# Kernel optimization log

Hardware: AMD Instinct MI355X
Metric: run time of the kernel (lower is better)

The kernel has to match this reference:

```python
import jax, jax.numpy as jnp
import numpy as np
import math

_OFFSETS = sorted(set(range(0, 33)) | {48, 64, 96, 128, 192, 256, 384, 512, 768, 1024, 1536})
B, N, D, H, FFN = 1, 2048, 1024, 16, 2816
EPS = 1e-6


def _rmsnorm(x, scale):
    rms = jnp.sqrt(jnp.mean(x * x, axis=-1, keepdims=True) + EPS)
    return scale * (x / rms)


def setup_inputs() -> dict:
    key = jax.random.key(0)
    ks = jax.random.split(key, 8)
    s = 0.02
    alphas = jnp.linspace(0.2, 2.0, H)
    delta_vals = jnp.array([math.log(1.0 + max(d, 0.2)) for d in _OFFSETS], dtype=jnp.float32)
    pos_bias = -delta_vals[:, None] * alphas[None, :]  # (n_offsets, H)
    return {
        "x": jax.random.normal(ks[0], (B, N, D), jnp.float32),
        "norm1_scale": jnp.ones((D,), jnp.float32),
        "norm2_scale": jnp.ones((D,), jnp.float32),
        "w_qkv": jax.random.normal(ks[1], (D, 3 * D), jnp.float32) * s,
        "w_out": jax.random.normal(ks[2], (D, D), jnp.float32) * s,
        "w_gate": jax.random.normal(ks[3], (D, D), jnp.float32) * s,
        "b_gate": jnp.full((D,), 2.0, jnp.float32),
        "pos_bias": pos_bias,
        "w_ffn_gate": jax.random.normal(ks[4], (D, FFN), jnp.float32) * s,
        "w_ffn_up": jax.random.normal(ks[5], (D, FFN), jnp.float32) * s,
        "w_ffn_down": jax.random.normal(ks[6], (FFN, D), jnp.float32) * s,
        "offsets": jnp.array(_OFFSETS, dtype=jnp.int32),
    }


def reference(x, norm1_scale, norm2_scale, w_qkv, w_out, w_gate, b_gate,
              pos_bias, w_ffn_gate, w_ffn_up, w_ffn_down, offsets):
    Bx, Nx, Dx = x.shape
    HD = Dx // H
    # --- attention branch: x + attn(norm1(x)) ---
    xn = _rmsnorm(x, norm1_scale)
    qkv = xn @ w_qkv
    q, k, v = jnp.split(qkv, 3, axis=-1)
    to_heads = lambda t: t.reshape(Bx, Nx, H, HD).transpose(0, 2, 1, 3)  # (B,H,N,HD)
    q, k, v = to_heads(q), to_heads(k), to_heads(v)

    t_idx = jnp.arange(Nx)
    # gather positions t-delta per (query t, offset o); clamped positions are masked below
    src = jnp.clip(t_idx[:, None] - offsets[None, :], 0, None)  # (N, O)
    Kg = k[:, :, src, :]  # (B,H,N,O,HD)
    Vg = v[:, :, src, :]

    scale = HD ** (-0.5)
    scores = jnp.einsum('bhnd,bhnod->bhno', q, Kg) * scale
    scores = scores + pos_bias.T[None, :, None, :]  # (1,H,1,O)
    invalid = t_idx[:, None] < offsets[None, :]      # (N, O)
    scores = jnp.where(invalid[None, None], -jnp.inf, scores)
    alpha = jax.nn.softmax(scores, axis=-1)
    out = jnp.einsum('bhno,bhnod->bhnd', alpha, Vg)
    out = out.transpose(0, 2, 1, 3).reshape(Bx, Nx, Dx)

    gate = jax.nn.sigmoid(xn @ w_gate + b_gate)
    x = x + (out * gate) @ w_out

    # --- FFN branch: x + SwiGLU(norm2(x)) ---
    xn2 = _rmsnorm(x, norm2_scale)
    x = x + (jax.nn.silu(xn2 @ w_ffn_gate) * (xn2 @ w_ffn_up)) @ w_ffn_down
    return x
```

## Files before the change

kernel.cpp:

```cpp
#include <hip/hip_runtime.h>
#include <hip/hip_bf16.h>
#include <math.h>

typedef __bf16 bf16;
typedef __bf16 v8bf __attribute__((ext_vector_type(8)));
typedef __bf16 v4bf __attribute__((ext_vector_type(4)));
typedef float v4f __attribute__((ext_vector_type(4)));

#define N_TOK 2048
#define DIM 1024
#define NH 16
#define FFN_DIM 2816

#define GLL(g, l) __builtin_amdgcn_global_load_lds(                         \
    (const __attribute__((address_space(1))) uint32_t*)(g),                 \
    (__attribute__((address_space(3))) uint32_t*)(l), 16, 0, 0)

#define WAITV(n) do {                                                        \
    switch (n) {                                                             \
    case 0: asm volatile("s_waitcnt vmcnt(0)" ::: "memory"); break;          \
    case 2: asm volatile("s_waitcnt vmcnt(2)" ::: "memory"); break;          \
    case 3: asm volatile("s_waitcnt vmcnt(3)" ::: "memory"); break;          \
    case 4: asm volatile("s_waitcnt vmcnt(4)" ::: "memory"); break;          \
    case 6: asm volatile("s_waitcnt vmcnt(6)" ::: "memory"); break;          \
    case 8: asm volatile("s_waitcnt vmcnt(8)" ::: "memory"); break;          \
    default: asm volatile("s_waitcnt vmcnt(0)" ::: "memory"); break; }       \
} while (0)

__global__ __launch_bounds__(256) void prep_all_kernel(
    const float* __restrict__ w_qkv, const float* __restrict__ w_gate,
    const float* __restrict__ w_out, const float* __restrict__ w_ffng,
    const float* __restrict__ w_ffnu, const float* __restrict__ w_ffnd,
    bf16* __restrict__ wqkvgT, bf16* __restrict__ woutT,
    bf16* __restrict__ wcatT, bf16* __restrict__ wffndT,
    const float* __restrict__ x, const float* __restrict__ n1s,
    bf16* __restrict__ xnb)
{
    int bid = blockIdx.x;
    const int tid = threadIdx.x;
    if (bid >= 13568) {
        int row = bid - 13568;
        float4 v = ((const float4*)(x + (size_t)row * DIM))[tid];
        float ss = v.x * v.x + v.y * v.y + v.z * v.z + v.w * v.w;
#pragma unroll
        for (int off = 32; off > 0; off >>= 1) ss += __shfl_down(ss, off);
        __shared__ float ps[4];
        if ((tid & 63) == 0) ps[tid >> 6] = ss;
        __syncthreads();
        float tot = ps[0] + ps[1] + ps[2] + ps[3];
        float inv = rsqrtf(tot * (1.0f / DIM) + 1e-6f);
        float4 s = ((const float4*)n1s)[tid];
        union { bf16 b[4]; uint2 u; } p;
        p.b[0] = (bf16)(v.x * inv * s.x);
        p.b[1] = (bf16)(v.y * inv * s.y);
        p.b[2] = (bf16)(v.z * inv * s.z);
        p.b[3] = (bf16)(v.w * inv * s.w);
        ((uint2*)(xnb + (size_t)row * DIM))[tid] = p.u;
        return;
    }
    const float* W; bf16* D; int Kd, Nc, nb, kb, dstbase;
    if (bid < 3072) {
        W = w_qkv; D = wqkvgT; Kd = 1024; Nc = 3072;
        nb = (bid % 96) * 32; kb = (bid / 96) * 32; dstbase = nb;
    } else if (bid < 4096) { int b = bid - 3072;
        W = w_gate; D = wqkvgT; Kd = 1024; Nc = 1024;
        nb = (b % 32) * 32; kb = (b / 32) * 32; dstbase = 3072 + nb;
    } else if (bid < 5120) { int b = bid - 4096;
        W = w_out; D = woutT; Kd = 1024; Nc = 1024;
        nb = (b % 32) * 32; kb = (b / 32) * 32; dstbase = nb;
    } else if (bid < 7936) { int b = bid - 5120;
        W = w_ffng; D = wcatT; Kd = 1024; Nc = 2816;
        nb = (b % 88) * 32; kb = (b / 88) * 32;
        dstbase = (nb >> 6) * 128 + (nb & 63);
    } else if (bid < 10752) { int b = bid - 7936;
        W = w_ffnu; D = wcatT; Kd = 1024; Nc = 2816;
        nb = (b % 88) * 32; kb = (b / 88) * 32;
        dstbase = (nb >> 6) * 128 + 64 + (nb & 63);
    } else { int b = bid - 10752;
        W = w_ffnd; D = wffndT; Kd = 2816; Nc = 1024;
        nb = (b % 32) * 32; kb = (b / 32) * 32; dstbase = nb;
    }
    __shared__ float tile[32][33];
    int tx = tid & 31, ty = tid >> 5;
#pragma unroll
    for (int r = 0; r < 4; ++r)
        tile[ty + r * 8][tx] = W[(size_t)(kb + ty + r * 8) * Nc + nb + tx];
    __syncthreads();
#pragma unroll
    for (int r = 0; r < 4; ++r)
        D[(size_t)(dstbase + ty + r * 8) * Kd + kb + tx] = (bf16)tile[tx][ty + r * 8];
}

__global__ __launch_bounds__(256) void rmsnorm_kernel(
    const float* __restrict__ x, const float* __restrict__ scale, bf16* __restrict__ out)
{
    int row = blockIdx.x, tid = threadIdx.x;
    float4 v = ((const float4*)(x + (size_t)row * DIM))[tid];
    float ss = v.x * v.x + v.y * v.y + v.z * v.z + v.w * v.w;
#pragma unroll
    for (int off = 32; off > 0; off >>= 1) ss += __shfl_down(ss, off);
    __shared__ float ps[4];
    if ((tid & 63) == 0) ps[tid >> 6] = ss;
    __syncthreads();
    float tot = ps[0] + ps[1] + ps[2] + ps[3];
    float inv = rsqrtf(tot * (1.0f / DIM) + 1e-6f);
    float4 s = ((const float4*)scale)[tid];
    union { bf16 b[4]; uint2 u; } p;
    p.b[0] = (bf16)(v.x * inv * s.x);
    p.b[1] = (bf16)(v.y * inv * s.y);
    p.b[2] = (bf16)(v.z * inv * s.z);
    p.b[3] = (bf16)(v.w * inv * s.w);
    ((uint2*)(out + (size_t)row * DIM))[tid] = p.u;
}

__global__ __launch_bounds__(256) void attn_kernel(
    const bf16* __restrict__ qkvg, const int* __restrict__ offs,
    const float* __restrict__ pos_bias, bf16* __restrict__ attgb)
{
    constexpr int O = 44;
    const int t = blockIdx.x, tid = threadIdx.x;
    const int wv = tid >> 6, lane = tid & 63;
    const int h1 = lane >> 2, l4 = lane & 3;
    const size_t RS = 4 * DIM;
    __shared__ float sS[O][17];
    __shared__ float sPB[O * 16];
    __shared__ int so[O];
    __shared__ float sAcc[4 * 1024];
    if (tid < O) so[tid] = offs[tid];
    for (int i = tid; i < O * 16; i += 256) sPB[i] = pos_bias[i];
    __syncthreads();

    const bf16* qbase = qkvg + (size_t)t * RS + h1 * 64;
    v8bf q0v = *(const v8bf*)(qbase + l4 * 8);
    v8bf q1v = *(const v8bf*)(qbase + 32 + l4 * 8);
    float qa[16];
#pragma unroll
    for (int e = 0; e < 8; ++e) {
        qa[e] = (float)q0v[e] * 0.125f;
        qa[8 + e] = (float)q1v[e] * 0.125f;
    }

#pragma unroll 4
    for (int it = 0; it < 11; ++it) {
        const int o = it * 4 + wv;
        const int src = t - so[o];
        const int srcc = src < 0 ? 0 : src;
        const bf16* kbase = qkvg + (size_t)srcc * RS + DIM + h1 * 64;
        v8bf k0 = *(const v8bf*)(kbase + l4 * 8);
        v8bf k1 = *(const v8bf*)(kbase + 32 + l4 * 8);
        float p = 0.f;
#pragma unroll
        for (int e = 0; e < 8; ++e) p += qa[e] * (float)k0[e];
#pragma unroll
        for (int e = 0; e < 8; ++e) p += qa[8 + e] * (float)k1[e];
        p += __shfl_xor(p, 1);
        p += __shfl_xor(p, 2);
        float s = (src >= 0) ? p + sPB[o * NH + h1] : -INFINITY;
        if (l4 == 0) sS[o][h1] = s;
    }
    __syncthreads();

    const int h = tid >> 4, j16 = tid & 15;
    float mx = -INFINITY;
#pragma unroll
    for (int o = j16; o < O; o += 16) mx = fmaxf(mx, sS[o][h]);
    mx = fmaxf(mx, __shfl_xor(mx, 1));
    mx = fmaxf(mx, __shfl_xor(mx, 2));
    mx = fmaxf(mx, __shfl_xor(mx, 4));
    mx = fmaxf(mx, __shfl_xor(mx, 8));
    float sum = 0.f;
#pragma unroll
    for (int o = j16; o < O; o += 16) {
        float e = __expf(sS[o][h] - mx);
        sS[o][h] = e;
        sum += e;
    }
    sum += __shfl_xor(sum, 1);
    sum += __shfl_xor(sum, 2);
    sum += __shfl_xor(sum, 4);
    sum += __shfl_xor(sum, 8);
    float inv = 1.0f / sum;
    __syncthreads();

    const int h2 = lane >> 2;
    const int dbase = lane * 16;
    float pacc[16] = {};
#pragma unroll 4
    for (int it = 0; it < 11; ++it) {
        int o = it * 4 + wv;
        int src = t - so[o];
        int srcc = src < 0 ? 0 : src;
        float a = sS[o][h2];
        const bf16* vb = qkvg + (size_t)srcc * RS + 2 * DIM + dbase;
        v8bf v0 = *(const v8bf*)(vb);
        v8bf v1 = *(const v8bf*)(vb + 8);
#pragma unroll
        for (int e = 0; e < 8; ++e) {
            pacc[e] += a * (float)v0[e];
            pacc[8 + e] += a * (float)v1[e];
        }
    }
#pragma unroll
    for (int q = 0; q < 4; ++q) {
        int phys = lane * 4 + (q ^ (lane & 3));
        *(float4*)&sAcc[wv * 1024 + phys * 4] =
            make_float4(pacc[q * 4], pacc[q * 4 + 1], pacc[q * 4 + 2], pacc[q * 4 + 3]);
    }
    __syncthreads();

    const int lr = tid >> 2, qr = tid & 3;
    const int phys = lr * 4 + (qr ^ (lr & 3));
    float4 p0 = *(const float4*)&sAcc[0 * 1024 + phys * 4];
    float4 p1 = *(const float4*)&sAcc[1 * 1024 + phys * 4];
    float4 p2 = *(const float4*)&sAcc[2 * 1024 + phys * 4];
    float4 p3 = *(const float4*)&sAcc[3 * 1024 + phys * 4];
    v4bf gv = *(const v4bf*)(qkvg + (size_t)t * RS + 3 * DIM + tid * 4);
    v4bf ov;
    ov[0] = (bf16)((p0.x + p1.x + p2.x + p3.x) * inv * (float)gv[0]);
    ov[1] = (bf16)((p0.y + p1.y + p2.y + p3.y) * inv * (float)gv[1]);
    ov[2] = (bf16)((p0.z + p1.z + p2.z + p3.z) * inv * (float)gv[2]);
    ov[3] = (bf16)((p0.w + p1.w + p2.w + p3.w) * inv * (float)gv[3]);
    *(v4bf*)(attgb + (size_t)t * DIM + tid * 4) = ov;
}

template<int BM, int BN, int NTHR, int NBUF, int EPI>
__global__ __launch_bounds__(NTHR) void gemm_kernel(
    const bf16* __restrict__ A, const bf16* __restrict__ Bt,
    int M, int N, int K,
    float* __restrict__ outf, bf16* __restrict__ outb,
    const float* __restrict__ e1, const float* __restrict__ bias)
{
    constexpr int WAVES = NTHR / 64;
    constexpr int WCOLS = WAVES / 2;
    constexpr int WME = BM / 2;
    constexpr int WNE = BN / WCOLS;
    constexpr int MI = WME / 16;
    constexpr int NJ = WNE / 16;
    constexpr int CH_A = BM * 4, CH_B = BN * 4;
    constexpr int LPT = (CH_A + CH_B) / NTHR;
    constexpr int STAGE_BYTES = NBUF * (BM + BN) * 32 * 2;
    constexpr int EPI_BYTES = (EPI == 6) ? BM * 66 * 4 : 0;
    constexpr int SMEM_BYTES = STAGE_BYTES > EPI_BYTES ? STAGE_BYTES : EPI_BYTES;
    __shared__ __align__(16) char smem[SMEM_BYTES];
    bf16* AsB = (bf16*)smem;
    bf16* BsB = (bf16*)(smem + NBUF * BM * 32 * 2);

    const int tid = threadIdx.x;
    const int m0 = blockIdx.y * BM, n0 = blockIdx.x * BN;
    const int lane = tid & 63, wave = tid >> 6;
    const int wr = wave / WCOLS, wc = wave % WCOLS;
    const int wm = wr * WME, wn = wc * WNE;
    const int lrow = lane & 15, l16 = lane >> 4;

    const bf16* gptr[LPT];
    int lo[LPT];
    bool pa[LPT];
#pragma unroll
    for (int i = 0; i < LPT; ++i) {
        int c = tid + i * NTHR;
        bool inA = c < CH_A;
        int cc = inA ? c : c - CH_A;
        int r = cc >> 2, q = cc & 3;
        int gq = (q ^ ((r >> 1) & 3)) * 8;
        gptr[i] = inA ? A + (size_t)(m0 + r) * K + gq
                      : Bt + (size_t)(n0 + r) * K + gq;
        lo[i] = r * 32 + q * 8;
        pa[i] = inA;
    }

    auto STAGE = [&](int b, int kt) {
        const int ko = kt * 32;
#pragma unroll
        for (int i = 0; i < LPT; ++i) {
            bf16* dst = (pa[i] ? AsB + b * BM * 32 : BsB + b * BN * 32) + lo[i];
            GLL(gptr[i] + ko, dst);
        }
    };

    v4f acc[MI][NJ] = {};
    const int NT = K >> 5;
#pragma unroll
    for (int i = 0; i < NBUF - 1; ++i) STAGE(i, i);

    for (int t = 0; t < NT; ++t) {
        const int rem = NT - 1 - t;
        const int wv_n = (rem < NBUF - 2 ? rem : NBUF - 2) * LPT;
        WAITV(wv_n);
        __builtin_amdgcn_s_barrier();
        __builtin_amdgcn_sched_barrier(0);
        const int b = t % NBUF;
        v8bf af[MI], bfr[NJ];
#pragma unroll
        for (int i = 0; i < MI; ++i) {
            int r = wm + i * 16 + lrow;
            af[i] = *(v8bf*)&AsB[b * BM * 32 + r * 32 + ((l16 ^ ((r >> 1) & 3)) * 8)];
        }
#pragma unroll
        for (int j = 0; j < NJ; ++j) {
            int r = wn + j * 16 + lrow;
            bfr[j] = *(v8bf*)&BsB[b * BN * 32 + r * 32 + ((l16 ^ ((r >> 1) & 3)) * 8)];
        }
        if (t + NBUF - 1 < NT) STAGE((t + NBUF - 1) % NBUF, t + NBUF - 1);
        __builtin_amdgcn_s_setprio(1);
#pragma unroll
        for (int i = 0; i < MI; ++i)
#pragma unroll
            for (int j = 0; j < NJ; ++j)
                acc[i][j] = __builtin_amdgcn_mfma_f32_16x16x32_bf16(af[i], bfr[j], acc[i][j], 0, 0, 0);
        __builtin_amdgcn_s_setprio(0);
    }

    if constexpr (EPI == 6) {
        float* eps = (float*)smem;
        const bool isGate = (wn < 64);
        asm volatile("s_waitcnt lgkmcnt(0)" ::: "memory");
        __builtin_amdgcn_s_barrier();
        if (isGate) {
#pragma unroll
            for (int i = 0; i < MI; ++i)
#pragma unroll
                for (int j = 0; j < NJ; ++j)
#pragma unroll
                    for (int r = 0; r < 4; ++r) {
                        int rowL = wm + i * 16 + l16 * 4 + r;
                        int colL = wn + j * 16 + lrow;
                        eps[rowL * 66 + colL] = acc[i][j][r];
                    }
        }
        asm volatile("s_waitcnt lgkmcnt(0)" ::: "memory");
        __builtin_amdgcn_s_barrier();
        if (!isGate) {
            const int halfN = N >> 1;
#pragma unroll
            for (int i = 0; i < MI; ++i)
#pragma unroll
                for (int j = 0; j < NJ; ++j)
#pragma unroll
                    for (int r = 0; r < 4; ++r) {
                        int rowL = wm + i * 16 + l16 * 4 + r;
                        int colU = wn - 64 + j * 16 + lrow;
                        float g = eps[rowL * 66 + colU];
                        float sil = g / (1.0f + __expf(-g));
                        float u = acc[i][j][r];
                        outb[(size_t)(m0 + rowL) * halfN + (n0 >> 1) + colU] = (bf16)(sil * u);
                    }
        }
        return;
    }

#pragma unroll
    for (int i = 0; i < MI; ++i)
#pragma unroll
        for (int j = 0; j < NJ; ++j)
#pragma unroll
            for (int r = 0; r < 4; ++r) {
                int row = m0 + wm + i * 16 + l16 * 4 + r;
                int col = n0 + wn + j * 16 + lrow;
                size_t idx = (size_t)row * N + col;
                float v = acc[i][j][r];
                if constexpr (EPI == 3) {
                    outf[idx] = e1[idx] + v;
                } else if constexpr (EPI == 5) {
                    if (col >= 3 * DIM) {
                        float g = 1.0f / (1.0f + __expf(-(v + bias[col - 3 * DIM])));
                        outb[idx] = (bf16)g;
                    } else {
                        outb[idx] = (bf16)v;
                    }
                }
            }
}

extern "C" void kernel_launch(void* const* d_in, const int* in_sizes, int n_in,
                              void* d_out, int out_size, void* d_ws, size_t ws_size,
                              hipStream_t stream)
{
    const float* x        = (const float*)d_in[0];
    const float* n1s      = (const float*)d_in[1];
    const float* n2s      = (const float*)d_in[2];
    const float* w_qkv    = (const float*)d_in[3];
    const float* w_out    = (const float*)d_in[4];
    const float* w_gate   = (const float*)d_in[5];
    const float* b_gate   = (const float*)d_in[6];
    const float* pos_bias = (const float*)d_in[7];
    const float* w_ffng   = (const float*)d_in[8];
    const float* w_ffnu   = (const float*)d_in[9];
    const float* w_ffnd   = (const float*)d_in[10];
    const int* offsets    = (const int*)d_in[11];
    float* out = (float*)d_out;

    char* ws = (char*)d_ws;
    size_t cur = 0;
    auto alloc = [&](size_t bytes) -> void* {
        void* p = ws + cur;
        cur += (bytes + 255) & ~(size_t)255;
        return p;
    };
    bf16*  xnb    = (bf16*)alloc((size_t)N_TOK * DIM * 2);
    bf16*  qkvgb  = (bf16*)alloc((size_t)N_TOK * 4 * DIM * 2);
    bf16*  attgb  = (bf16*)alloc((size_t)N_TOK * DIM * 2);
    float* x1     = (float*)alloc((size_t)N_TOK * DIM * 4);
    bf16*  xn2b   = (bf16*)alloc((size_t)N_TOK * DIM * 2);
    bf16*  hb     = (bf16*)alloc((size_t)N_TOK * FFN_DIM * 2);
    bf16*  wqkvgT = (bf16*)alloc((size_t)4 * DIM * DIM * 2);
    bf16*  woutT  = (bf16*)alloc((size_t)DIM * DIM * 2);
    bf16*  wcatT  = (bf16*)alloc((size_t)2 * FFN_DIM * DIM * 2);
    bf16*  wffndT = (bf16*)alloc((size_t)FFN_DIM * DIM * 2);

    prep_all_kernel<<<13568 + N_TOK, 256, 0, stream>>>(
        w_qkv, w_gate, w_out, w_ffng, w_ffnu, w_ffnd,
        wqkvgT, woutT, wcatT, wffndT, x, n1s, xnb);

    gemm_kernel<128, 128, 256, 3, 5><<<dim3(32, 16), 256, 0, stream>>>(
        xnb, wqkvgT, N_TOK, 4 * DIM, DIM, nullptr, qkvgb, nullptr, b_gate);
    attn_kernel<<<dim3(N_TOK), 256, 0, stream>>>(qkvgb, offsets, pos_bias, attgb);
    gemm_kernel<64, 64, 256, 6, 3><<<dim3(16, 32), 256, 0, stream>>>(
        attgb, woutT, N_TOK, DIM, DIM, x1, nullptr, x, nullptr);
    rmsnorm_kernel<<<N_TOK, 256, 0, stream>>>(x1, n2s, xn2b);
    gemm_kernel<128, 128, 256, 3, 6><<<dim3(44, 16), 256, 0, stream>>>(
        xn2b, wcatT, N_TOK, 2 * FFN_DIM, DIM, nullptr, hb, nullptr, nullptr);
    gemm_kernel<64, 64, 256, 6, 3><<<dim3(16, 32), 256, 0, stream>>>(
        hb, wffndT, N_TOK, DIM, FFN_DIM, out, nullptr, x1, nullptr);
}
```

Baseline: 159.5 us.

## Add 512-thread BK=64 GEMM for QKV and FFN up-projections

Adds a new GEMM kernel with 8 waves per block, K-tile of 64 with an XOR-swizzled LDS layout, and a triple-buffered pipeline that splits each prefetch into two halves interleaved with the MFMA work. It replaces the 256-thread BK=32 GEMM for the QKV+gate and fused SwiGLU up-projections. The aim is fewer barriers per K, more waves to hide latency, and better LDS reuse, in exchange for higher LDS use (96KB) that may reduce occupancy. The EPI 5/6 epilogues move into the new kernel and are removed from the old one.

```diff
diff --git a/kernel.cpp b/kernel.cpp
--- a/kernel.cpp
+++ b/kernel.cpp
@@ -20,7 +20,6 @@
     switch (n) {                                                             \
     case 0: asm volatile("s_waitcnt vmcnt(0)" ::: "memory"); break;          \
     case 2: asm volatile("s_waitcnt vmcnt(2)" ::: "memory"); break;          \
-    case 3: asm volatile("s_waitcnt vmcnt(3)" ::: "memory"); break;          \
     case 4: asm volatile("s_waitcnt vmcnt(4)" ::: "memory"); break;          \
     case 6: asm volatile("s_waitcnt vmcnt(6)" ::: "memory"); break;          \
     case 8: asm volatile("s_waitcnt vmcnt(8)" ::: "memory"); break;          \
@@ -223,6 +222,149 @@
     *(v4bf*)(attgb + (size_t)t * DIM + tid * 4) = ov;
 }
 
+template<int EPI>
+__global__ __launch_bounds__(512) void gemm2p_kernel(
+    const bf16* __restrict__ A, const bf16* __restrict__ Bt,
+    int M, int N, int K,
+    bf16* __restrict__ outb, const float* __restrict__ bias)
+{
+    constexpr int BM = 128, BN = 128, BK = 64, NBUF = 3;
+    constexpr int MI = 4, NJ = 2;
+    __shared__ __align__(16) char smem[NBUF * (BM + BN) * BK * 2];
+    bf16* AsB = (bf16*)smem;
+    bf16* BsB = (bf16*)(smem + NBUF * BM * BK * 2);
+
+    const int tid = threadIdx.x;
+    const int m0 = blockIdx.y * BM, n0 = blockIdx.x * BN;
+    const int lane = tid & 63, wave = tid >> 6;
+    const int wr = wave >> 2, wc = wave & 3;
+    const int wm = wr * 64, wn = wc * 32;
+    const int lrow = lane & 15, l16 = lane >> 4;
+
+    const bf16* gptr[4];
+    int lo[4];
+    bool pa_[4];
+#pragma unroll
+    for (int i = 0; i < 4; ++i) {
+        int c = tid + i * 512;
+        bool inA = c < 1024;
+        int cc = inA ? c : c - 1024;
+        int r = cc >> 3, q = cc & 7;
+        int gq = (q ^ (r & 7)) * 8;
+        gptr[i] = inA ? A + (size_t)(m0 + r) * K + gq
+                      : Bt + (size_t)(n0 + r) * K + gq;
+        lo[i] = r * BK + q * 8;
+        pa_[i] = inA;
+    }
+
+    auto STAGE2 = [&](int b, int kt, int i0) {
+#pragma unroll
+        for (int i = 0; i < 2; ++i) {
+            int ii = i0 + i;
+            bf16* dst = (pa_[ii] ? AsB + b * BM * BK : BsB + b * BN * BK) + lo[ii];
+            GLL(gptr[ii] + kt * BK, dst);
+        }
+    };
+
+    v4f acc[MI][NJ] = {};
+    const int NT = K / BK;
+    STAGE2(0, 0, 0); STAGE2(0, 0, 2);
+    STAGE2(1, 1, 0); STAGE2(1, 1, 2);
+
+    for (int t = 0; t < NT; ++t) {
+        if (t < NT - 1) WAITV(4);
+        else            WAITV(0);
+        __builtin_amdgcn_s_barrier();
+        __builtin_amdgcn_sched_barrier(0);
+        const int b = t % NBUF;
+        const int bp = (t + 2) % NBUF;
+        const bool pf = (t + 2) < NT;
+#pragma unroll
+        for (int h = 0; h < 2; ++h) {
+            if (pf) STAGE2(bp, t + 2, h * 2);
+            v8bf af[MI], bfr[NJ];
+#pragma unroll
+            for (int i = 0; i < MI; ++i) {
+                int r = wm + i * 16 + lrow;
+                int ch = (h * 4 + l16) ^ (r & 7);
+                af[i] = *(v8bf*)&AsB[b * BM * BK + r * BK + ch * 8];
+            }
+#pragma unroll
+            for (int j = 0; j < NJ; ++j) {
+                int r = wn + j * 16 + lrow;
+                int ch = (h * 4 + l16) ^ (r & 7);
+                bfr[j] = *(v8bf*)&BsB[b * BN * BK + r * BK + ch * 8];
+            }
+            __builtin_amdgcn_s_setprio(1);
+#pragma unroll
+            for (int i = 0; i < MI; ++i)
+#pragma unroll
+                for (int j = 0; j < NJ; ++j)
+                    acc[i][j] = __builtin_amdgcn_mfma_f32_16x16x32_bf16(af[i], bfr[j], acc[i][j], 0, 0, 0);
+            __builtin_amdgcn_s_setprio(0);
+        }
+        __builtin_amdgcn_s_barrier();
+    }
+
+    if constexpr (EPI == 6) {
+        float* eps = (float*)smem;
+        const bool isGate = (wn < 64);
+        asm volatile("s_waitcnt lgkmcnt(0)" ::: "memory");
+        __builtin_amdgcn_s_barrier();
+        if (isGate) {
+#pragma unroll
+            for (int i = 0; i < MI; ++i)
+#pragma unroll
+                for (int j = 0; j < NJ; ++j)
+#pragma unroll
+                    for (int r = 0; r < 4; ++r) {
+                        int rowL = wm + i * 16 + l16 * 4 + r;
+                        int colL = wn + j * 16 + lrow;
+                        eps[rowL * 66 + colL] = acc[i][j][r];
+                    }
+        }
+        asm volatile("s_waitcnt lgkmcnt(0)" ::: "memory");
+        __builtin_amdgcn_s_barrier();
+        if (!isGate) {
+            const int halfN = N >> 1;
+#pragma unroll
+            for (int i = 0; i < MI; ++i)
+#pragma unroll
+                for (int j = 0; j < NJ; ++j)
+#pragma unroll
+                    for (int r = 0; r < 4; ++r) {
+                        int rowL = wm + i * 16 + l16 * 4 + r;
+                        int colU = wn - 64 + j * 16 + lrow;
+                        float g = eps[rowL * 66 + colU];
+                        float sil = g / (1.0f + __expf(-g));
+                        float u = acc[i][j][r];
+                        outb[(size_t)(m0 + rowL) * halfN + (n0 >> 1) + colU] = (bf16)(sil * u);
+                    }
+        }
+        return;
+    }
+
+#pragma unroll
+    for (int i = 0; i < MI; ++i)
+#pragma unroll
+        for (int j = 0; j < NJ; ++j)
+#pragma unroll
+            for (int r = 0; r < 4; ++r) {
+                int row = m0 + wm + i * 16 + l16 * 4 + r;
+                int col = n0 + wn + j * 16 + lrow;
+                size_t idx = (size_t)row * N + col;
+                float v = acc[i][j][r];
+                if constexpr (EPI == 5) {
+                    if (col >= 3 * DIM) {
+                        float g = 1.0f / (1.0f + __expf(-(v + bias[col - 3 * DIM])));
+                        outb[idx] = (bf16)g;
+                    } else {
+                        outb[idx] = (bf16)v;
+                    }
+                }
+            }
+}
+
 template<int BM, int BN, int NTHR, int NBUF, int EPI>
 __global__ __launch_bounds__(NTHR) void gemm_kernel(
     const bf16* __restrict__ A, const bf16* __restrict__ Bt,
@@ -238,10 +380,7 @@
     constexpr int NJ = WNE / 16;
     constexpr int CH_A = BM * 4, CH_B = BN * 4;
     constexpr int LPT = (CH_A + CH_B) / NTHR;
-    constexpr int STAGE_BYTES = NBUF * (BM + BN) * 32 * 2;
-    constexpr int EPI_BYTES = (EPI == 6) ? BM * 66 * 4 : 0;
-    constexpr int SMEM_BYTES = STAGE_BYTES > EPI_BYTES ? STAGE_BYTES : EPI_BYTES;
-    __shared__ __align__(16) char smem[SMEM_BYTES];
+    __shared__ __align__(16) char smem[NBUF * (BM + BN) * 32 * 2];
     bf16* AsB = (bf16*)smem;
     bf16* BsB = (bf16*)(smem + NBUF * BM * 32 * 2);
 
@@ -310,44 +449,6 @@
         __builtin_amdgcn_s_setprio(0);
     }
 
-    if constexpr (EPI == 6) {
-        float* eps = (float*)smem;
-        const bool isGate = (wn < 64);
-        asm volatile("s_waitcnt lgkmcnt(0)" ::: "memory");
-        __builtin_amdgcn_s_barrier();
-        if (isGate) {
-#pragma unroll
-            for (int i = 0; i < MI; ++i)
-#pragma unroll
-                for (int j = 0; j < NJ; ++j)
-#pragma unroll
-                    for (int r = 0; r < 4; ++r) {
-                        int rowL = wm + i * 16 + l16 * 4 + r;
-                        int colL = wn + j * 16 + lrow;
-                        eps[rowL * 66 + colL] = acc[i][j][r];
-                    }
-        }
-        asm volatile("s_waitcnt lgkmcnt(0)" ::: "memory");
-        __builtin_amdgcn_s_barrier();
-        if (!isGate) {
-            const int halfN = N >> 1;
-#pragma unroll
-            for (int i = 0; i < MI; ++i)
-#pragma unroll
-                for (int j = 0; j < NJ; ++j)
-#pragma unroll
-                    for (int r = 0; r < 4; ++r) {
-                        int rowL = wm + i * 16 + l16 * 4 + r;
-                        int colU = wn - 64 + j * 16 + lrow;
-                        float g = eps[rowL * 66 + colU];
-                        float sil = g / (1.0f + __expf(-g));
-                        float u = acc[i][j][r];
-                        outb[(size_t)(m0 + rowL) * halfN + (n0 >> 1) + colU] = (bf16)(sil * u);
-                    }
-        }
-        return;
-    }
-
 #pragma unroll
     for (int i = 0; i < MI; ++i)
 #pragma unroll
@@ -360,13 +461,6 @@
                 float v = acc[i][j][r];
                 if constexpr (EPI == 3) {
                     outf[idx] = e1[idx] + v;
-                } else if constexpr (EPI == 5) {
-                    if (col >= 3 * DIM) {
-                        float g = 1.0f / (1.0f + __expf(-(v + bias[col - 3 * DIM])));
-                        outb[idx] = (bf16)g;
-                    } else {
-                        outb[idx] = (bf16)v;
-                    }
                 }
             }
 }
@@ -411,14 +505,14 @@
         w_qkv, w_gate, w_out, w_ffng, w_ffnu, w_ffnd,
         wqkvgT, woutT, wcatT, wffndT, x, n1s, xnb);
 
-    gemm_kernel<128, 128, 256, 3, 5><<<dim3(32, 16), 256, 0, stream>>>(
-        xnb, wqkvgT, N_TOK, 4 * DIM, DIM, nullptr, qkvgb, nullptr, b_gate);
+    gemm2p_kernel<5><<<dim3(32, 16), 512, 0, stream>>>(
+        xnb, wqkvgT, N_TOK, 4 * DIM, DIM, qkvgb, b_gate);
     attn_kernel<<<dim3(N_TOK), 256, 0, stream>>>(qkvgb, offsets, pos_bias, attgb);
     gemm_kernel<64, 64, 256, 6, 3><<<dim3(16, 32), 256, 0, stream>>>(
         attgb, woutT, N_TOK, DIM, DIM, x1, nullptr, x, nullptr);
     rmsnorm_kernel<<<N_TOK, 256, 0, stream>>>(x1, n2s, xn2b);
-    gemm_kernel<128, 128, 256, 3, 6><<<dim3(44, 16), 256, 0, stream>>>(
-        xn2b, wcatT, N_TOK, 2 * FFN_DIM, DIM, nullptr, hb, nullptr, nullptr);
+    gemm2p_kernel<6><<<dim3(44, 16), 512, 0, stream>>>(
+        xn2b, wcatT, N_TOK, 2 * FFN_DIM, DIM, hb, nullptr);
     gemm_kernel<64, 64, 256, 6, 3><<<dim3(16, 32), 256, 0, stream>>>(
         hb, wffndT, N_TOK, DIM, FFN_DIM, out, nullptr, x1, nullptr);
 }
```

New measurement: 163.7 us. 1.03x slower.
